# Optimization experiments

Measured on AMD Instinct MI355X. Metric: run time of the kernel, lower is better.

## Reference

```python
import jax, jax.numpy as jnp
import numpy as np

B, S, H, DH = 2, 2048, 16, 64
D = H * DH


def setup_inputs() -> dict:
    key = jax.random.key(0)
    ks = jax.random.split(key, 10)
    std = 0.02
    return {
        "hidden_states": jax.random.normal(ks[0], (B, S, D), jnp.float32),
        "mask": jax.random.randint(ks[1], (B, S), 0, 2, jnp.int64 if jax.config.jax_enable_x64 else jnp.int32),
        "Wq": jax.random.normal(ks[2], (D, D), jnp.float32) * std,
        "bq": jnp.zeros((D,), jnp.float32),
        "Wk": jax.random.normal(ks[3], (D, D), jnp.float32) * std,
        "bk": jnp.zeros((D,), jnp.float32),
        "Wv": jax.random.normal(ks[4], (D, D), jnp.float32) * std,
        "bv": jnp.zeros((D,), jnp.float32),
        "Wo": jax.random.normal(ks[5], (D, D), jnp.float32) * std,
        "bo": jnp.zeros((D,), jnp.float32),
    }


def _split_heads(x):
    # (B, S, H*DH) -> (B, H, S, DH)
    b, s, _ = x.shape
    return x.reshape(b, s, H, DH).transpose(0, 2, 1, 3)


def reference(hidden_states, mask, Wq, bq, Wk, bk, Wv, bv, Wo, bo):
    # Linear projections (torch nn.Linear: x @ W.T + b)
    q = _split_heads(hidden_states @ Wq.T + bq)
    k = _split_heads(hidden_states @ Wk.T + bk)
    v = _split_heads(hidden_states @ Wv.T + bv)

    scale = 1.0 / np.sqrt(DH).astype(np.float32)
    scores = jnp.einsum("bhqd,bhkd->bhqk", q, k) * scale  # (B,H,S,S)
    # mask out padded key positions (mask==0 -> -inf), broadcast over heads/queries
    scores = jnp.where(mask[:, None, None, :] == 0, -jnp.inf, scores)
    weights = jax.nn.softmax(scores, axis=-1)

    attended = jnp.einsum("bhqk,bhkd->bhqd", weights, v)  # (B,H,S,DH)
    merged = attended.transpose(0, 2, 1, 3).reshape(hidden_states.shape)  # (B,S,D)
    return merged @ Wo.T + bo
```

## Files before the change

kernel.cpp:

```cpp
#include <hip/hip_runtime.h>
#include <hip/hip_bf16.h>

typedef __bf16 bf16;
typedef __bf16 bf16x4 __attribute__((ext_vector_type(4)));
typedef __bf16 bf16x8 __attribute__((ext_vector_type(8)));
typedef float f32x4 __attribute__((ext_vector_type(4)));

#define B_ 2
#define S_ 2048
#define H_ 16
#define DH_ 64
#define D_ 1024
#define NT_ 4096

#define WAIT_VMCNT0() asm volatile("s_waitcnt vmcnt(0)" ::: "memory")
#define WAIT_LGKM0()  asm volatile("s_waitcnt lgkmcnt(0)" ::: "memory")

__device__ __forceinline__ void gld_lds16(const bf16* g, bf16* l) {
    __builtin_amdgcn_global_load_lds(
        (__attribute__((address_space(1))) void*)g,
        (__attribute__((address_space(3))) void*)l, 16, 0, 0);
}

__device__ __forceinline__ bf16 f2bf(float x) {
    union { float f; unsigned u; } v; v.f = x;
    unsigned short h = (unsigned short)((v.u + 0x7FFF + ((v.u >> 16) & 1)) >> 16);
    return __builtin_bit_cast(bf16, h);
}

__global__ __launch_bounds__(256) void cvt_kernel(
    const float* __restrict__ hs,
    const float* __restrict__ Wq, const float* __restrict__ Wk,
    const float* __restrict__ Wv, const float* __restrict__ Wo,
    bf16* __restrict__ hsb, bf16* __restrict__ wqkv, bf16* __restrict__ wob)
{
    int i = (blockIdx.x * 256 + threadIdx.x) * 4;
    const float* src;
    bf16* dst;
    if (i < 4194304) {
        src = hs + i; dst = hsb + i;
    } else if (i < 7340032) {
        int off = i - 4194304;
        int which = off >> 20;
        int within = off & 1048575;
        src = (which == 0 ? Wq : which == 1 ? Wk : Wv) + within;
        dst = wqkv + off;
    } else {
        int off = i - 7340032;
        src = Wo + off; dst = wob + off;
    }
    float4 v = *(const float4*)src;
    bf16x4 o = { (bf16)v.x, (bf16)v.y, (bf16)v.z, (bf16)v.w };
    *(bf16x4*)dst = o;
}

__global__ __launch_bounds__(256, 3) void gemm_bt(
    const bf16* __restrict__ A, const bf16* __restrict__ Bm,
    int mode,
    const float* __restrict__ b0, const float* __restrict__ b1,
    const float* __restrict__ b2,
    bf16* __restrict__ Qo, bf16* __restrict__ Ko, bf16* __restrict__ Vt,
    float* __restrict__ Co)
{
    const int K = 1024;
    __shared__ __attribute__((aligned(16))) bf16 sA[128 * 64];
    __shared__ __attribute__((aligned(16))) bf16 sB[128 * 64];

    int tid = threadIdx.x;
    int wave = tid >> 6, lane = tid & 63;
    int quad = lane >> 4, l16 = lane & 15;
    int m0 = blockIdx.x * 128;
    int n0 = blockIdx.y * 128;
    int wm = (wave & 1) * 64, wn = (wave >> 1) * 64;
    int fs = l16 & 7;

    f32x4 acc[4][4];
#pragma unroll
    for (int i = 0; i < 4; i++)
#pragma unroll
        for (int j = 0; j < 4; j++) acc[i][j] = (f32x4){0.f, 0.f, 0.f, 0.f};

    for (int k0 = 0; k0 < K; k0 += 64) {
#pragma unroll
        for (int i = 0; i < 4; i++) {
            int c = tid + i * 256;
            int row = c >> 3;
            int kc = ((c & 7) ^ (row & 7)) * 8;
            gld_lds16(A + (size_t)(m0 + row) * K + k0 + kc, &sA[c * 8]);
            gld_lds16(Bm + (size_t)(n0 + row) * K + k0 + kc, &sB[c * 8]);
        }
        WAIT_VMCNT0();
        __syncthreads();

#pragma unroll
        for (int kp = 0; kp < 2; kp++) {
            bf16x8 af[4], bfr[4];
#pragma unroll
            for (int i = 0; i < 4; i++)
                af[i] = *(const bf16x8*)&sA[(wm + i * 16 + l16) * 64 + (((kp * 4 + quad) ^ fs) * 8)];
#pragma unroll
            for (int j = 0; j < 4; j++)
                bfr[j] = *(const bf16x8*)&sB[(wn + j * 16 + l16) * 64 + (((kp * 4 + quad) ^ fs) * 8)];
#pragma unroll
            for (int i = 0; i < 4; i++)
#pragma unroll
                for (int j = 0; j < 4; j++)
                    acc[i][j] = __builtin_amdgcn_mfma_f32_16x16x32_bf16(
                        af[i], bfr[j], acc[i][j], 0, 0, 0);
        }
        __syncthreads();
    }

    if (mode == 0) {
        const float QSCALE = 0.125f * 1.44269504088896340736f;
#pragma unroll
        for (int j = 0; j < 4; j++) {
            int n = n0 + wn + j * 16 + l16;
            int region = n >> 10;
            int nn = n & 1023;
            int h = nn >> 6, d = nn & 63;
            float bias = (region == 0 ? b0 : region == 1 ? b1 : b2)[nn];
#pragma unroll
            for (int i = 0; i < 4; i++)
#pragma unroll
                for (int r = 0; r < 4; r++) {
                    int m = m0 + wm + i * 16 + quad * 4 + r;
                    int b = m >> 11, s = m & 2047;
                    int bh = b * H_ + h;
                    float v = acc[i][j][r] + bias;
                    if (region == 0)
                        Qo[((size_t)bh * S_ + s) * DH_ + d] = f2bf(v * QSCALE);
                    else if (region == 1)
                        Ko[((size_t)bh * S_ + s) * DH_ + d] = f2bf(v);
                    else
                        Vt[((size_t)bh * DH_ + d) * S_ + s] = f2bf(v);
                }
        }
    } else {
#pragma unroll
        for (int j = 0; j < 4; j++) {
            int n = n0 + wn + j * 16 + l16;
            float bias = b0[n];
#pragma unroll
            for (int i = 0; i < 4; i++)
#pragma unroll
                for (int r = 0; r < 4; r++) {
                    int m = m0 + wm + i * 16 + quad * 4 + r;
                    Co[(size_t)m * D_ + n] = acc[i][j][r] + bias;
                }
        }
    }
}

__global__ __launch_bounds__(256, 2) void attn_kernel(
    const bf16* __restrict__ Q, const bf16* __restrict__ Kg,
    const bf16* __restrict__ Vt, const int* __restrict__ mask,
    bf16* __restrict__ Og)
{
    __shared__ __attribute__((aligned(16))) bf16 sK[128 * 64];
    __shared__ __attribute__((aligned(16))) bf16 sV[64 * 128];
    __shared__ __attribute__((aligned(16))) bf16 sP[4][64 * 40];
    __shared__ float sMaddAll[S_];
    __shared__ float sPsumR[128];
    __shared__ float sPsumF[128];

    int tid = threadIdx.x;
    int wave = tid >> 6, lane = tid & 63;
    int quad = lane >> 4, l16 = lane & 15;
    int bh = blockIdx.y;
    int b = bh >> 4;
    int q0 = blockIdx.x * 128;
    int f8 = l16 & 7;
    int qh = wave & 1;
    int kh = wave >> 1;

    const bf16* Qb = Q + (size_t)bh * S_ * DH_;
    const bf16* Kb = Kg + (size_t)bh * S_ * DH_;
    const bf16* Vb = Vt + (size_t)bh * DH_ * S_;

#pragma unroll
    for (int i = 0; i < S_ / 256; i++) {
        int idx = tid + i * 256;
        sMaddAll[idx] = mask[b * S_ + idx] ? 0.f : -1e30f;
    }

    bf16x8 aq[4][2];
#pragma unroll
    for (int qt = 0; qt < 4; qt++) {
        int qrow = q0 + qh * 64 + qt * 16 + l16;
        aq[qt][0] = *(const bf16x8*)&Qb[(size_t)qrow * DH_ + quad * 8];
        aq[qt][1] = *(const bf16x8*)&Qb[(size_t)qrow * DH_ + 32 + quad * 8];
    }

    f32x4 o[4][4];
#pragma unroll
    for (int i = 0; i < 4; i++)
#pragma unroll
        for (int j = 0; j < 4; j++) o[i][j] = (f32x4){0.f, 0.f, 0.f, 0.f};
    float psum[4] = {0.f, 0.f, 0.f, 0.f};

    for (int kt = 0; kt < S_; kt += 128) {
#pragma unroll
        for (int i = 0; i < 8; i++) {
            int c = tid + i * 256;
            if (c < 1024) {
                int row = c >> 3;
                int g = (c & 7) ^ (row & 7);
                gld_lds16(&Kb[(size_t)(kt + row) * DH_ + g * 8], &sK[c * 8]);
            } else {
                int cv = c - 1024;
                int row = cv >> 4;
                int g = (cv & 15) ^ (row & 15);
                gld_lds16(&Vb[(size_t)row * S_ + kt + g * 8], &sV[cv * 8]);
            }
        }
        WAIT_VMCNT0();
        __syncthreads();

#pragma unroll
        for (int pass = 0; pass < 2; pass++) {
#pragma unroll
            for (int mtl = 0; mtl < 2; mtl++) {
                int keyrow = kh * 64 + pass * 32 + mtl * 16;
                bf16x8 ak0 = *(const bf16x8*)&sK[(keyrow + l16) * 64 + (quad ^ f8) * 8];
                bf16x8 ak1 = *(const bf16x8*)&sK[(keyrow + l16) * 64 + ((quad + 4) ^ f8) * 8];
                float4 ma4 = *(const float4*)&sMaddAll[kt + keyrow + quad * 4];
#pragma unroll
                for (int qt = 0; qt < 4; qt++) {
                    f32x4 c = (f32x4){0.f, 0.f, 0.f, 0.f};
                    c = __builtin_amdgcn_mfma_f32_16x16x32_bf16(ak0, aq[qt][0], c, 0, 0, 0);
                    c = __builtin_amdgcn_mfma_f32_16x16x32_bf16(ak1, aq[qt][1], c, 0, 0, 0);
                    float p0 = __builtin_amdgcn_exp2f(c[0] + ma4.x);
                    float p1 = __builtin_amdgcn_exp2f(c[1] + ma4.y);
                    float p2 = __builtin_amdgcn_exp2f(c[2] + ma4.z);
                    float p3 = __builtin_amdgcn_exp2f(c[3] + ma4.w);
                    psum[qt] += (p0 + p1) + (p2 + p3);
                    bf16x4 pk = { f2bf(p0), f2bf(p1), f2bf(p2), f2bf(p3) };
                    *(bf16x4*)&sP[wave][(qt * 16 + l16) * 40 + (mtl * 4 + quad) * 4] = pk;
                }
            }

            WAIT_LGKM0();
            bf16x8 ap[4];
#pragma unroll
            for (int qt = 0; qt < 4; qt++)
                ap[qt] = *(const bf16x8*)&sP[wave][(qt * 16 + l16) * 40 + quad * 8];
#pragma unroll
            for (int dt = 0; dt < 4; dt++) {
                int g = (kh * 8 + pass * 4 + quad) ^ l16;
                bf16x8 bv = *(const bf16x8*)&sV[(dt * 16 + l16) * 128 + g * 8];
#pragma unroll
                for (int qt = 0; qt < 4; qt++)
                    o[qt][dt] = __builtin_amdgcn_mfma_f32_16x16x32_bf16(ap[qt], bv, o[qt][dt], 0, 0, 0);
            }
        }
        __syncthreads();
    }

#pragma unroll
    for (int qt = 0; qt < 4; qt++) {
        float v = psum[qt];
        v += __shfl_xor(v, 16);
        v += __shfl_xor(v, 32);
        psum[qt] = v;
    }

    __syncthreads();
    float* sRed = (wave == 2) ? (float*)sK : (float*)sV;
    if (wave >= 2) {
#pragma unroll
        for (int qt = 0; qt < 4; qt++)
#pragma unroll
            for (int dt = 0; dt < 4; dt++)
                *(f32x4*)&sRed[((qt * 4 + dt) * 64 + lane) * 4] = o[qt][dt];
#pragma unroll
        for (int qt = 0; qt < 4; qt++)
            sPsumR[(wave - 2) * 64 + qt * 16 + l16] = psum[qt];
    }
    __syncthreads();
    if (wave < 2) {
        float* src = (wave == 0) ? (float*)sK : (float*)sV;
#pragma unroll
        for (int qt = 0; qt < 4; qt++)
#pragma unroll
            for (int dt = 0; dt < 4; dt++)
                o[qt][dt] += *(const f32x4*)&src[((qt * 4 + dt) * 64 + lane) * 4];
#pragma unroll
        for (int qt = 0; qt < 4; qt++) {
            float v = psum[qt] + sPsumR[wave * 64 + qt * 16 + l16];
            sPsumF[wave * 64 + qt * 16 + l16] = v;
        }
        WAIT_LGKM0();
        int h = bh & 15;
#pragma unroll
        for (int qt = 0; qt < 4; qt++) {
            float4 ps = *(const float4*)&sPsumF[wave * 64 + qt * 16 + quad * 4];
            float rcp[4] = { 1.f / ps.x, 1.f / ps.y, 1.f / ps.z, 1.f / ps.w };
#pragma unroll
            for (int r = 0; r < 4; r++) {
                int s = q0 + qh * 64 + qt * 16 + quad * 4 + r;
#pragma unroll
                for (int dt = 0; dt < 4; dt++) {
                    int d = dt * 16 + l16;
                    Og[((size_t)(b * S_ + s)) * D_ + h * 64 + d] = f2bf(o[qt][dt][r] * rcp[r]);
                }
            }
        }
    }
}

extern "C" void kernel_launch(void* const* d_in, const int* in_sizes, int n_in,
                              void* d_out, int out_size, void* d_ws, size_t ws_size,
                              hipStream_t stream) {
    const float* hs = (const float*)d_in[0];
    const int* mask = (const int*)d_in[1];
    const float* Wq = (const float*)d_in[2];
    const float* bq = (const float*)d_in[3];
    const float* Wk = (const float*)d_in[4];
    const float* bk = (const float*)d_in[5];
    const float* Wv = (const float*)d_in[6];
    const float* bv = (const float*)d_in[7];
    const float* Wo = (const float*)d_in[8];
    const float* bo = (const float*)d_in[9];
    float* out = (float*)d_out;

    char* ws = (char*)d_ws;
    bf16* hsb  = (bf16*)(ws);
    bf16* wqkv = (bf16*)(ws + ((size_t)8 << 20));
    bf16* wob  = (bf16*)(ws + ((size_t)14 << 20));
    bf16* Qw   = (bf16*)(ws + ((size_t)16 << 20));
    bf16* Kw   = (bf16*)(ws + ((size_t)24 << 20));
    bf16* Vtw  = (bf16*)(ws + ((size_t)32 << 20));
    bf16* attn = (bf16*)(ws + ((size_t)40 << 20));

    cvt_kernel<<<8192, 256, 0, stream>>>(hs, Wq, Wk, Wv, Wo, hsb, wqkv, wob);
    gemm_bt<<<dim3(32, 24), 256, 0, stream>>>(hsb, wqkv, 0, bq, bk, bv,
                                              Qw, Kw, Vtw, nullptr);
    attn_kernel<<<dim3(16, 32), 256, 0, stream>>>(Qw, Kw, Vtw, mask, attn);
    gemm_bt<<<dim3(32, 8), 256, 0, stream>>>(attn, wob, 1, bo, nullptr, nullptr,
                                             nullptr, nullptr, nullptr, out);
}
```

Baseline: 205.9 us.

## Split output projection into smaller-tile GEMM and vectorize V-transpose stores

The output projection moves to a dedicated kernel with 128x64 tiles, which doubles the grid to 512 blocks so more of the GPU's compute units are busy. The QKV projection drops its mode branch, and the transposed V epilogue now packs four consecutive sequence values into one 8-byte store instead of four scalar stores. Smaller tiles mean more redundant loading of A across blocks and less MFMA work per LDS load.

```diff
diff --git a/kernel.cpp b/kernel.cpp
--- a/kernel.cpp
+++ b/kernel.cpp
@@ -56,11 +56,9 @@
 
 __global__ __launch_bounds__(256, 3) void gemm_bt(
     const bf16* __restrict__ A, const bf16* __restrict__ Bm,
-    int mode,
     const float* __restrict__ b0, const float* __restrict__ b1,
     const float* __restrict__ b2,
-    bf16* __restrict__ Qo, bf16* __restrict__ Ko, bf16* __restrict__ Vt,
-    float* __restrict__ Co)
+    bf16* __restrict__ Qo, bf16* __restrict__ Ko, bf16* __restrict__ Vt)
 {
     const int K = 1024;
     __shared__ __attribute__((aligned(16))) bf16 sA[128 * 64];
@@ -111,44 +109,107 @@
         __syncthreads();
     }
 
-    if (mode == 0) {
-        const float QSCALE = 0.125f * 1.44269504088896340736f;
-#pragma unroll
-        for (int j = 0; j < 4; j++) {
-            int n = n0 + wn + j * 16 + l16;
-            int region = n >> 10;
-            int nn = n & 1023;
-            int h = nn >> 6, d = nn & 63;
-            float bias = (region == 0 ? b0 : region == 1 ? b1 : b2)[nn];
-#pragma unroll
-            for (int i = 0; i < 4; i++)
+    const float QSCALE = 0.125f * 1.44269504088896340736f;
+#pragma unroll
+    for (int j = 0; j < 4; j++) {
+        int n = n0 + wn + j * 16 + l16;
+        int region = n >> 10;
+        int nn = n & 1023;
+        int h = nn >> 6, d = nn & 63;
+        float bias = (region == 0 ? b0 : region == 1 ? b1 : b2)[nn];
+#pragma unroll
+        for (int i = 0; i < 4; i++) {
+            int mb = m0 + wm + i * 16 + quad * 4;
+            int b = mb >> 11, s = mb & 2047;
+            int bh = b * H_ + h;
+            if (region == 2) {
+                bf16x4 pk = { f2bf(acc[i][j][0] + bias), f2bf(acc[i][j][1] + bias),
+                              f2bf(acc[i][j][2] + bias), f2bf(acc[i][j][3] + bias) };
+                *(bf16x4*)&Vt[((size_t)bh * DH_ + d) * S_ + s] = pk;
+            } else {
 #pragma unroll
                 for (int r = 0; r < 4; r++) {
-                    int m = m0 + wm + i * 16 + quad * 4 + r;
-                    int b = m >> 11, s = m & 2047;
-                    int bh = b * H_ + h;
                     float v = acc[i][j][r] + bias;
                     if (region == 0)
-                        Qo[((size_t)bh * S_ + s) * DH_ + d] = f2bf(v * QSCALE);
-                    else if (region == 1)
-                        Ko[((size_t)bh * S_ + s) * DH_ + d] = f2bf(v);
+                        Qo[((size_t)bh * S_ + s + r) * DH_ + d] = f2bf(v * QSCALE);
                     else
-                        Vt[((size_t)bh * DH_ + d) * S_ + s] = f2bf(v);
+                        Ko[((size_t)bh * S_ + s + r) * DH_ + d] = f2bf(v);
                 }
-        }
-    } else {
-#pragma unroll
-        for (int j = 0; j < 4; j++) {
-            int n = n0 + wn + j * 16 + l16;
-            float bias = b0[n];
+            }
+        }
+    }
+}
+
+__global__ __launch_bounds__(256, 2) void gemm_out(
+    const bf16* __restrict__ A, const bf16* __restrict__ Bm,
+    const float* __restrict__ bias0, float* __restrict__ Co)
+{
+    const int K = 1024;
+    __shared__ __attribute__((aligned(16))) bf16 sA[128 * 64];
+    __shared__ __attribute__((aligned(16))) bf16 sB[64 * 64];
+
+    int tid = threadIdx.x;
+    int wave = tid >> 6, lane = tid & 63;
+    int quad = lane >> 4, l16 = lane & 15;
+    int m0 = blockIdx.x * 128;
+    int n0 = blockIdx.y * 64;
+    int wm = (wave & 1) * 64, wn = (wave >> 1) * 32;
+    int fs = l16 & 7;
+
+    f32x4 acc[4][2];
+#pragma unroll
+    for (int i = 0; i < 4; i++)
+#pragma unroll
+        for (int j = 0; j < 2; j++) acc[i][j] = (f32x4){0.f, 0.f, 0.f, 0.f};
+
+    for (int k0 = 0; k0 < K; k0 += 64) {
+#pragma unroll
+        for (int i = 0; i < 4; i++) {
+            int c = tid + i * 256;
+            int row = c >> 3;
+            int kc = ((c & 7) ^ (row & 7)) * 8;
+            gld_lds16(A + (size_t)(m0 + row) * K + k0 + kc, &sA[c * 8]);
+        }
+#pragma unroll
+        for (int i = 0; i < 2; i++) {
+            int c = tid + i * 256;
+            int row = c >> 3;
+            int kc = ((c & 7) ^ (row & 7)) * 8;
+            gld_lds16(Bm + (size_t)(n0 + row) * K + k0 + kc, &sB[c * 8]);
+        }
+        WAIT_VMCNT0();
+        __syncthreads();
+
+#pragma unroll
+        for (int kp = 0; kp < 2; kp++) {
+            bf16x8 af[4], bfr[2];
 #pragma unroll
             for (int i = 0; i < 4; i++)
-#pragma unroll
-                for (int r = 0; r < 4; r++) {
-                    int m = m0 + wm + i * 16 + quad * 4 + r;
-                    Co[(size_t)m * D_ + n] = acc[i][j][r] + bias;
-                }
-        }
+                af[i] = *(const bf16x8*)&sA[(wm + i * 16 + l16) * 64 + (((kp * 4 + quad) ^ fs) * 8)];
+#pragma unroll
+            for (int j = 0; j < 2; j++)
+                bfr[j] = *(const bf16x8*)&sB[(wn + j * 16 + l16) * 64 + (((kp * 4 + quad) ^ fs) * 8)];
+#pragma unroll
+            for (int i = 0; i < 4; i++)
+#pragma unroll
+                for (int j = 0; j < 2; j++)
+                    acc[i][j] = __builtin_amdgcn_mfma_f32_16x16x32_bf16(
+                        af[i], bfr[j], acc[i][j], 0, 0, 0);
+        }
+        __syncthreads();
+    }
+
+#pragma unroll
+    for (int j = 0; j < 2; j++) {
+        int n = n0 + wn + j * 16 + l16;
+        float bias = bias0[n];
+#pragma unroll
+        for (int i = 0; i < 4; i++)
+#pragma unroll
+            for (int r = 0; r < 4; r++) {
+                int m = m0 + wm + i * 16 + quad * 4 + r;
+                Co[(size_t)m * D_ + n] = acc[i][j][r] + bias;
+            }
     }
 }
 
@@ -334,9 +395,8 @@
     bf16* attn = (bf16*)(ws + ((size_t)40 << 20));
 
     cvt_kernel<<<8192, 256, 0, stream>>>(hs, Wq, Wk, Wv, Wo, hsb, wqkv, wob);
-    gemm_bt<<<dim3(32, 24), 256, 0, stream>>>(hsb, wqkv, 0, bq, bk, bv,
-                                              Qw, Kw, Vtw, nullptr);
+    gemm_bt<<<dim3(32, 24), 256, 0, stream>>>(hsb, wqkv, bq, bk, bv,
+                                              Qw, Kw, Vtw);
     attn_kernel<<<dim3(16, 32), 256, 0, stream>>>(Qw, Kw, Vtw, mask, attn);
-    gemm_bt<<<dim3(32, 8), 256, 0, stream>>>(attn, wob, 1, bo, nullptr, nullptr,
-                                             nullptr, nullptr, nullptr, out);
-}
+    gemm_out<<<dim3(32, 16), 256, 0, stream>>>(attn, wob, bo, out);
+}
```

Measured after the change: 197.0 us. 1.05x faster.
